# Kernel tuning notes

Measured on AMD Instinct MI355X. Metric: run time of the kernel, lower is better.

Reference implementation:

```python
import jax, jax.numpy as jnp
import numpy as np

B, L, E, V = 4, 2048, 1024, 64
NT = V * (V - 1) // 2  # 2016 upper-triangular entries
LN_EPS = 1e-5


def setup_inputs() -> dict:
    key = jax.random.key(0)
    ks = jax.random.split(key, 9)
    s = lambda d: 1.0 / np.sqrt(d)
    return {
        "hx": jax.random.normal(ks[0], (B, L, E), dtype=jnp.float32),
        "W_dense": jax.random.normal(ks[1], (E, E), dtype=jnp.float32) * s(E),
        "b_dense": jnp.zeros((E,), dtype=jnp.float32),
        "ln_g": jnp.ones((E,), dtype=jnp.float32),
        "ln_b": jnp.zeros((E,), dtype=jnp.float32),
        "W_theta": jax.random.normal(ks[2], (V, E), dtype=jnp.float32) * s(E),
        "b_theta": jnp.zeros((V,), dtype=jnp.float32),
        "W_Theta": jax.random.normal(ks[3], (NT, E), dtype=jnp.float32) * s(E),
        "b_Theta": jnp.zeros((NT,), dtype=jnp.float32),
    }


def reference(hx, W_dense, b_dense, ln_g, ln_b, W_theta, b_theta, W_Theta, b_Theta):
    # dense -> exact (erf) gelu -> LayerNorm (ESM1bLayerNorm)
    h = jax.nn.gelu(hx @ W_dense.T + b_dense, approximate=False)
    mu = jnp.mean(h, axis=-1, keepdims=True)
    var = jnp.mean(jnp.square(h - mu), axis=-1, keepdims=True)
    h = (h - mu) / jnp.sqrt(var + LN_EPS) * ln_g + ln_b

    pi = jax.nn.softmax(h @ W_theta.T + b_theta, axis=-1)          # (B,L,V)
    Theta = jax.nn.softplus(h @ W_Theta.T + b_Theta)               # (B,L,NT)

    iu, ju = np.triu_indices(V, k=1)
    S = jnp.zeros((B, L, V, V), dtype=h.dtype).at[:, :, iu, ju].set(Theta)
    S = S + jnp.swapaxes(S, -2, -1)                                # symmetric, zero diag

    # diag(1/sqrt(pi)) @ S @ diag(sqrt(pi)) == S * sqrt(pi_j)/sqrt(pi_i)
    pi_sqrt = jnp.sqrt(pi)
    Q = S * (pi_sqrt[..., None, :] / pi_sqrt[..., :, None])
    Q = Q - Q.sum(axis=-1)[..., :, None] * jnp.eye(V, dtype=Q.dtype)
    return (Q, pi)
```

## Files before the change

### kernel.cpp

```cpp
#include <hip/hip_runtime.h>
#include <hip/hip_bf16.h>
#include <cstdint>
#include <cstddef>

#define MROWS 8192
#define EDIM  1024
#define VDIM  64
#define NTRI  2016
#define NTC   2176

typedef _Float16 half8  __attribute__((ext_vector_type(8)));
typedef _Float16 half4v __attribute__((ext_vector_type(4)));
typedef float    floatx4 __attribute__((ext_vector_type(4)));

typedef __attribute__((address_space(1))) void gvoid;
typedef __attribute__((address_space(3))) void svoid;

__device__ inline void gld_lds16(const _Float16* g, _Float16* l) {
    __builtin_amdgcn_global_load_lds((gvoid*)g, (svoid*)l, 16, 0, 0);
}

__device__ inline float fast_erf(float x) {
    float ax = fabsf(x);
    float t = 1.0f / (1.0f + 0.3275911f * ax);
    float p = t * (0.254829592f +
              t * (-0.284496736f +
              t * (1.421413741f +
              t * (-1.453152027f +
              t * 1.061405429f))));
    float r = 1.0f - p * __expf(-ax * ax);
    return copysignf(r, x);
}

__device__ inline float fast_softplus(float x) {
    return fmaxf(x, 0.0f) + __logf(1.0f + __expf(-fabsf(x)));
}

__global__ __launch_bounds__(256) void cast_f2h(const float* __restrict__ in,
                                                _Float16* __restrict__ out,
                                                int n_valid, int n_total) {
    int idx = (blockIdx.x * 256 + threadIdx.x) * 4;
    if (idx >= n_total) return;
    half4v o;
    if (idx < n_valid) {
        float4 v = *(const float4*)(in + idx);
        o[0] = (_Float16)v.x; o[1] = (_Float16)v.y;
        o[2] = (_Float16)v.z; o[3] = (_Float16)v.w;
    } else {
        o[0] = (_Float16)0.f; o[1] = (_Float16)0.f;
        o[2] = (_Float16)0.f; o[3] = (_Float16)0.f;
    }
    *(half4v*)(out + idx) = o;
}

template <int MODE>
__global__ __launch_bounds__(256) void gemm_bt(const _Float16* __restrict__ A,
                                               const _Float16* __restrict__ Bt,
                                               const float* __restrict__ bias,
                                               const float* __restrict__ bias2,
                                               float* __restrict__ C, int N) {
    __shared__ __align__(16) _Float16 As[128 * 32];
    __shared__ __align__(16) _Float16 Bs[128 * 32];

    const int tid  = threadIdx.x;
    const int n0   = blockIdx.x * 128;
    const int m0   = blockIdx.y * 128;
    const int w    = tid >> 6;
    const int lane = tid & 63;
    const int wr   = w >> 1;
    const int wc   = w & 1;
    const int lrow  = lane & 15;
    const int lquad = lane >> 4;

    floatx4 acc[4][4] = {};

    const int r0  = tid >> 2;
    const int sw0 = (r0 >> 1) & 3;
    const int kk0 = ((tid & 3) ^ sw0) * 8;
    const _Float16* Ag0 = A  + (size_t)(m0 + r0) * EDIM + kk0;
    const _Float16* Ag1 = Ag0 + (size_t)64 * EDIM;
    const _Float16* Bg0 = Bt + (size_t)(n0 + r0) * EDIM + kk0;
    const _Float16* Bg1 = Bg0 + (size_t)64 * EDIM;
    _Float16* As0 = &As[tid * 8];
    _Float16* As1 = As0 + 2048;
    _Float16* Bs0 = &Bs[tid * 8];
    _Float16* Bs1 = Bs0 + 2048;

    const int swr = (lrow >> 1) & 3;
    const _Float16* ardA = &As[(wr * 64 + lrow) * 32 + ((lquad ^ swr) * 8)];
    const _Float16* brdB = &Bs[(wc * 64 + lrow) * 32 + ((lquad ^ swr) * 8)];

    for (int k0 = 0; k0 < EDIM; k0 += 32) {
        gld_lds16(Ag0 + k0, As0);
        gld_lds16(Ag1 + k0, As1);
        gld_lds16(Bg0 + k0, Bs0);
        gld_lds16(Bg1 + k0, Bs1);
        __syncthreads();

        half8 af[4], bf[4];
#pragma unroll
        for (int t = 0; t < 4; ++t) {
            af[t] = *(const half8*)(ardA + t * 16 * 32);
            bf[t] = *(const half8*)(brdB + t * 16 * 32);
        }
#pragma unroll
        for (int i = 0; i < 4; ++i)
#pragma unroll
            for (int j = 0; j < 4; ++j)
                acc[i][j] = __builtin_amdgcn_mfma_f32_16x16x32_f16(
                    af[i], bf[j], acc[i][j], 0, 0, 0);
        __syncthreads();
    }

    const int cm = m0 + wr * 64 + lquad * 4;
    const int cn = n0 + wc * 64 + lrow;
#pragma unroll
    for (int j = 0; j < 4; ++j) {
        const int gn = cn + j * 16;
        float bv;
        if (MODE == 0) {
            bv = bias[gn];
        } else {
            if (gn < NTRI)            bv = bias[gn];
            else if (gn < NTRI + VDIM) bv = bias2[gn - NTRI];
            else                      bv = 0.0f;
        }
#pragma unroll
        for (int i = 0; i < 4; ++i) {
#pragma unroll
            for (int r = 0; r < 4; ++r) {
                float x = acc[i][j][r] + bv;
                float y;
                if (MODE == 0) {
                    y = 0.5f * x * (1.0f + fast_erf(x * 0.70710678118654752f));
                } else {
                    if (gn < NTRI) {
                        y = fast_softplus(x);
                    } else if (gn < NTRI + VDIM) {
                        y = x;
                    } else {
                        y = 0.0f;
                    }
                }
                C[(size_t)(cm + i * 16 + r) * N + gn] = y;
            }
        }
    }
}

__global__ __launch_bounds__(256) void ln_kernel(float* __restrict__ H,
                                                 const float* __restrict__ gw,
                                                 const float* __restrict__ bw,
                                                 _Float16* __restrict__ Hh) {
    const int row = blockIdx.x, tid = threadIdx.x;
    float4 v = ((const float4*)(H + (size_t)row * EDIM))[tid];
    float s  = v.x + v.y + v.z + v.w;
    float ss = v.x * v.x + v.y * v.y + v.z * v.z + v.w * v.w;
#pragma unroll
    for (int off = 32; off; off >>= 1) {
        s  += __shfl_down(s, off);
        ss += __shfl_down(ss, off);
    }
    __shared__ float red[8];
    const int w = tid >> 6, lane = tid & 63;
    if (lane == 0) { red[w] = s; red[4 + w] = ss; }
    __syncthreads();
    const float st  = red[0] + red[1] + red[2] + red[3];
    const float sst = red[4] + red[5] + red[6] + red[7];
    const float mu  = st * (1.0f / EDIM);
    const float rs  = 1.0f / sqrtf(sst * (1.0f / EDIM) - mu * mu + 1e-5f);
    float4 gg = ((const float4*)gw)[tid];
    float4 bb = ((const float4*)bw)[tid];
    float4 y;
    y.x = (v.x - mu) * rs * gg.x + bb.x;
    y.y = (v.y - mu) * rs * gg.y + bb.y;
    y.z = (v.z - mu) * rs * gg.z + bb.z;
    y.w = (v.w - mu) * rs * gg.w + bb.w;
    ((float4*)(H + (size_t)row * EDIM))[tid] = y;
    half4v h4;
    h4[0] = (_Float16)y.x; h4[1] = (_Float16)y.y;
    h4[2] = (_Float16)y.z; h4[3] = (_Float16)y.w;
    ((half4v*)(Hh + (size_t)row * EDIM))[tid] = h4;
}

__global__ __launch_bounds__(256) void softmax_kernel(const float* __restrict__ Theta,
                                                      float* __restrict__ pi_out,
                                                      float* __restrict__ sp) {
    const int lane = threadIdx.x & 63;
    const int row  = blockIdx.x * 4 + (threadIdx.x >> 6);
    float lg = Theta[(size_t)row * NTC + NTRI + lane];
    float m = lg;
#pragma unroll
    for (int off = 32; off; off >>= 1) m = fmaxf(m, __shfl_xor(m, off));
    float e = __expf(lg - m);
    float ssum = e;
#pragma unroll
    for (int off = 32; off; off >>= 1) ssum += __shfl_xor(ssum, off);
    float p = e / ssum;
    pi_out[(size_t)row * VDIM + lane] = p;
    sp[(size_t)row * VDIM + lane] = sqrtf(p);
}

__global__ __launch_bounds__(256) void q_kernel(const float* __restrict__ Theta,
                                                const float* __restrict__ sp,
                                                float* __restrict__ Q) {
    const int row = blockIdx.x;
    __shared__ float Th[NTRI];
    __shared__ float spv[VDIM];
    const float* trow = Theta + (size_t)row * NTC;
    for (int t = threadIdx.x; t < NTRI; t += 256) Th[t] = trow[t];
    if (threadIdx.x < VDIM) spv[threadIdx.x] = sp[(size_t)row * VDIM + threadIdx.x];
    __syncthreads();

    const int i = threadIdx.x >> 2;
    const int q = threadIdx.x & 3;
    const float rpi = 1.0f / spv[i];
    float vals[16];
    float psum = 0.f;
#pragma unroll
    for (int c = 0; c < 16; ++c) {
        const int j = q * 16 + c;
        float out = 0.f;
        if (j != i) {
            const int a = (i < j) ? i : j;
            const int b = (i < j) ? j : i;
            const int t = a * (127 - a) / 2 + (b - a - 1);
            out = Th[t] * spv[j] * rpi;
            psum += out;
        }
        vals[c] = out;
    }
    psum += __shfl_xor(psum, 1);
    psum += __shfl_xor(psum, 2);

    float* qrow = Q + ((size_t)row * VDIM + i) * VDIM + q * 16;
    float4* dst = (float4*)qrow;
    dst[0] = make_float4(vals[0], vals[1], vals[2], vals[3]);
    dst[1] = make_float4(vals[4], vals[5], vals[6], vals[7]);
    dst[2] = make_float4(vals[8], vals[9], vals[10], vals[11]);
    dst[3] = make_float4(vals[12], vals[13], vals[14], vals[15]);
    if ((i >> 4) == q) {
        Q[((size_t)row * VDIM + i) * VDIM + i] = -psum;
    }
}

extern "C" void kernel_launch(void* const* d_in, const int* in_sizes, int n_in,
                              void* d_out, int out_size, void* d_ws, size_t ws_size,
                              hipStream_t stream) {
    const float* hx      = (const float*)d_in[0];
    const float* W_dense = (const float*)d_in[1];
    const float* b_dense = (const float*)d_in[2];
    const float* ln_g    = (const float*)d_in[3];
    const float* ln_b    = (const float*)d_in[4];
    const float* W_theta = (const float*)d_in[5];
    const float* b_theta = (const float*)d_in[6];
    const float* W_Theta = (const float*)d_in[7];
    const float* b_Theta = (const float*)d_in[8];

    uint8_t* ws = (uint8_t*)d_ws;
    _Float16* A_h  = (_Float16*)ws;
    _Float16* Wd_h = (_Float16*)(ws + (size_t)16 * 1048576);
    _Float16* Wc_h = (_Float16*)(ws + (size_t)18 * 1048576);
    float*    G    = (float*)(ws + (size_t)23 * 1048576);
    float*    Theta= (float*)(ws + (size_t)23 * 1048576);
    float*    sp   = (float*)(ws + (size_t)92 * 1048576);

    float* Q_out  = (float*)d_out;
    float* pi_out = (float*)d_out + (size_t)MROWS * VDIM * VDIM;

    cast_f2h<<<(MROWS * EDIM / 4) / 256, 256, 0, stream>>>(hx, A_h, MROWS * EDIM, MROWS * EDIM);
    cast_f2h<<<(EDIM * EDIM / 4) / 256, 256, 0, stream>>>(W_dense, Wd_h, EDIM * EDIM, EDIM * EDIM);
    cast_f2h<<<(NTRI * EDIM / 4) / 256, 256, 0, stream>>>(W_Theta, Wc_h, NTRI * EDIM, NTRI * EDIM);
    cast_f2h<<<((NTC - NTRI) * EDIM / 4) / 256, 256, 0, stream>>>(
        W_theta, Wc_h + (size_t)NTRI * EDIM, VDIM * EDIM, (NTC - NTRI) * EDIM);

    gemm_bt<0><<<dim3(EDIM / 128, MROWS / 128), 256, 0, stream>>>(
        A_h, Wd_h, b_dense, nullptr, G, EDIM);

    ln_kernel<<<MROWS, 256, 0, stream>>>(G, ln_g, ln_b, A_h);

    gemm_bt<1><<<dim3(NTC / 128, MROWS / 128), 256, 0, stream>>>(
        A_h, Wc_h, b_Theta, b_theta, Theta, NTC);

    softmax_kernel<<<MROWS / 4, 256, 0, stream>>>(Theta, pi_out, sp);

    q_kernel<<<MROWS, 256, 0, stream>>>(Theta, sp, Q_out);
}
```

Measured before the change: 371.2 us.

## Deepen GEMM K-tile to 64 and remap blocks for XCD-local L2 reuse

Raises the GEMM K-step from 32 to 64, so each barrier pair now covers two MFMA k-substeps. This halves the number of __syncthreads and load-issue rounds, and the LDS swizzle is widened to 8 chunks to match. It also replaces the 2D grid with a 1D grid whose block index is split by XCD, so blocks on the same XCD share M row-tiles and get better L2 locality. LDS use doubles to 32KB per block, which may lower occupancy, and there is still no double buffering.

```diff
diff --git a/kernel.cpp b/kernel.cpp
--- a/kernel.cpp
+++ b/kernel.cpp
@@ -59,12 +59,18 @@
                                                const float* __restrict__ bias,
                                                const float* __restrict__ bias2,
                                                float* __restrict__ C, int N) {
-    __shared__ __align__(16) _Float16 As[128 * 32];
-    __shared__ __align__(16) _Float16 Bs[128 * 32];
+    __shared__ __align__(16) _Float16 As[128 * 64];
+    __shared__ __align__(16) _Float16 Bs[128 * 64];
 
     const int tid  = threadIdx.x;
-    const int n0   = blockIdx.x * 128;
-    const int m0   = blockIdx.y * 128;
+    const int ng   = N >> 7;
+    const int xcd  = blockIdx.x & 7;
+    const int slot = blockIdx.x >> 3;
+    const int mg   = slot / ng;
+    const int nn   = slot - mg * ng;
+    const int m0   = (xcd + mg * 8) * 128;
+    const int n0   = nn * 128;
+
     const int w    = tid >> 6;
     const int lane = tid & 63;
     const int wr   = w >> 1;
@@ -74,41 +80,47 @@
 
     floatx4 acc[4][4] = {};
 
-    const int r0  = tid >> 2;
-    const int sw0 = (r0 >> 1) & 3;
-    const int kk0 = ((tid & 3) ^ sw0) * 8;
-    const _Float16* Ag0 = A  + (size_t)(m0 + r0) * EDIM + kk0;
-    const _Float16* Ag1 = Ag0 + (size_t)64 * EDIM;
-    const _Float16* Bg0 = Bt + (size_t)(n0 + r0) * EDIM + kk0;
-    const _Float16* Bg1 = Bg0 + (size_t)64 * EDIM;
-    _Float16* As0 = &As[tid * 8];
-    _Float16* As1 = As0 + 2048;
-    _Float16* Bs0 = &Bs[tid * 8];
-    _Float16* Bs1 = Bs0 + 2048;
-
-    const int swr = (lrow >> 1) & 3;
-    const _Float16* ardA = &As[(wr * 64 + lrow) * 32 + ((lquad ^ swr) * 8)];
-    const _Float16* brdB = &Bs[(wc * 64 + lrow) * 32 + ((lquad ^ swr) * 8)];
-
-    for (int k0 = 0; k0 < EDIM; k0 += 32) {
-        gld_lds16(Ag0 + k0, As0);
-        gld_lds16(Ag1 + k0, As1);
-        gld_lds16(Bg0 + k0, Bs0);
-        gld_lds16(Bg1 + k0, Bs1);
+    const int r0 = tid >> 3;
+    const int c0 = tid & 7;
+    const int g  = (c0 ^ (r0 & 7)) * 8;
+    const _Float16* Ag[4];
+    const _Float16* Bg[4];
+#pragma unroll
+    for (int call = 0; call < 4; ++call) {
+        Ag[call] = A  + (size_t)(m0 + call * 32 + r0) * EDIM + g;
+        Bg[call] = Bt + (size_t)(n0 + call * 32 + r0) * EDIM + g;
+    }
+    _Float16* AsD = &As[tid * 8];
+    _Float16* BsD = &Bs[tid * 8];
+
+    const int swr = lrow & 7;
+    const _Float16* ardA = &As[(wr * 64 + lrow) * 64];
+    const _Float16* brdB = &Bs[(wc * 64 + lrow) * 64];
+
+    for (int k0 = 0; k0 < EDIM; k0 += 64) {
+#pragma unroll
+        for (int call = 0; call < 4; ++call) {
+            gld_lds16(Ag[call] + k0, AsD + call * 2048);
+            gld_lds16(Bg[call] + k0, BsD + call * 2048);
+        }
         __syncthreads();
 
-        half8 af[4], bf[4];
-#pragma unroll
-        for (int t = 0; t < 4; ++t) {
-            af[t] = *(const half8*)(ardA + t * 16 * 32);
-            bf[t] = *(const half8*)(brdB + t * 16 * 32);
-        }
-#pragma unroll
-        for (int i = 0; i < 4; ++i)
-#pragma unroll
-            for (int j = 0; j < 4; ++j)
-                acc[i][j] = __builtin_amdgcn_mfma_f32_16x16x32_f16(
-                    af[i], bf[j], acc[i][j], 0, 0, 0);
+#pragma unroll
+        for (int kstep = 0; kstep < 2; ++kstep) {
+            const int soff = ((kstep * 4 + lquad) ^ swr) * 8;
+            half8 af[4], bf[4];
+#pragma unroll
+            for (int t = 0; t < 4; ++t) {
+                af[t] = *(const half8*)(ardA + t * 16 * 64 + soff);
+                bf[t] = *(const half8*)(brdB + t * 16 * 64 + soff);
+            }
+#pragma unroll
+            for (int i = 0; i < 4; ++i)
+#pragma unroll
+                for (int j = 0; j < 4; ++j)
+                    acc[i][j] = __builtin_amdgcn_mfma_f32_16x16x32_f16(
+                        af[i], bf[j], acc[i][j], 0, 0, 0);
+        }
         __syncthreads();
     }
 
@@ -121,9 +133,9 @@
         if (MODE == 0) {
             bv = bias[gn];
         } else {
-            if (gn < NTRI)            bv = bias[gn];
+            if (gn < NTRI)             bv = bias[gn];
             else if (gn < NTRI + VDIM) bv = bias2[gn - NTRI];
-            else                      bv = 0.0f;
+            else                       bv = 0.0f;
         }
 #pragma unroll
         for (int i = 0; i < 4; ++i) {
@@ -274,12 +286,12 @@
     cast_f2h<<<((NTC - NTRI) * EDIM / 4) / 256, 256, 0, stream>>>(
         W_theta, Wc_h + (size_t)NTRI * EDIM, VDIM * EDIM, (NTC - NTRI) * EDIM);
 
-    gemm_bt<0><<<dim3(EDIM / 128, MROWS / 128), 256, 0, stream>>>(
+    gemm_bt<0><<<(EDIM / 128) * (MROWS / 128), 256, 0, stream>>>(
         A_h, Wd_h, b_dense, nullptr, G, EDIM);
 
     ln_kernel<<<MROWS, 256, 0, stream>>>(G, ln_g, ln_b, A_h);
 
-    gemm_bt<1><<<dim3(NTC / 128, MROWS / 128), 256, 0, stream>>>(
+    gemm_bt<1><<<(NTC / 128) * (MROWS / 128), 256, 0, stream>>>(
         A_h, Wc_h, b_Theta, b_theta, Theta, NTC);
 
     softmax_kernel<<<MROWS / 4, 256, 0, stream>>>(Theta, pi_out, sp);
```

After: 352.2 us. 5.1% less time.
